# Performance work log

Measured on AMD Instinct MI355X. Metric: run time of the kernel, lower is better.

Reference implementation:

```python
import jax, jax.numpy as jnp
import numpy as np

# --- constants from loss_param_dict (fallback norm_info: means=0, stds=1 -> denorm is identity) ---
A_DIV, A_NS, A_BC = 0.3, 0.3, 0.3
A_LOSS = 1.0 - A_DIV - A_NS - A_BC
SCALE_BASE, SCALE_DIV, SCALE_NS, SCALE_BC = 300000.0, 1e-05, 0.01, 1.0
SX, SY = 1.2 / 127, 0.8 / 127  # spacing along axis 2 (x) and axis 1 (y)
RHO, MU = 1.0, 1.0
H, W = 128, 128
IN_TOP = H // 2 + H // 16 + 1  # 73
IN_BOT = H // 2 - H // 16 - 1  # 55
NORM_MEAN = np.array([0.0, 0.0, 0.0, 0.0], dtype=np.float32)
NORM_STD = np.array([1.0, 1.0, 1.0, 1.0], dtype=np.float32)


def grad_axis(f, h, axis):
    """torch.gradient: 2nd-order central interior, 1st-order one-sided edges."""
    f = jnp.moveaxis(f, axis, -1)
    left = (f[..., 1:2] - f[..., 0:1]) / h
    interior = (f[..., 2:] - f[..., :-2]) / (2.0 * h)
    right = (f[..., -1:] - f[..., -2:-1]) / h
    g = jnp.concatenate([left, interior, right], axis=-1)
    return jnp.moveaxis(g, -1, axis)


def setup_inputs() -> dict:
    key = jax.random.key(0)
    k1, k2, k3 = jax.random.split(key, 3)
    B = 256
    return {
        "inputs": jax.random.normal(k1, (B, 1, H, W), dtype=jnp.float32),
        "outputs": jax.random.normal(k2, (B, 3, H, W), dtype=jnp.float32),
        "targets": jax.random.normal(k3, (B, 3, H, W), dtype=jnp.float32),
    }


def reference(inputs, outputs, targets):
    # base MSE loss (reduction='sum')
    loss_base = jnp.sum((outputs - targets) ** 2) / SCALE_BASE

    # denormalisation (norm_info fallback: identity, but kept for faithfulness)
    in_ch = inputs.shape[1]
    mean = jnp.asarray(NORM_MEAN)
    std = jnp.asarray(NORM_STD)
    inp = inputs * std[:in_ch][None, :, None, None] + mean[:in_ch][None, :, None, None]
    out = outputs * std[in_ch:][None, :, None, None] + mean[in_ch:][None, :, None, None]

    # boundary residual pieces (on full, un-cropped denormalised outputs)
    pieces = [
        out[:, 1, IN_BOT:IN_TOP, 0].ravel() - 0.01,
        out[:, 0, IN_BOT:IN_TOP, -1].ravel(),
    ]
    for ch in (1, 2):
        for idx in (0, -1):
            pieces += [
                out[:, ch, idx, :].ravel(),
                out[:, ch, IN_TOP:, idx].ravel(),
                out[:, ch, 0:IN_BOT, idx].ravel(),
            ]
    boundary = jnp.concatenate(pieces)

    # interior crop [B, C, 126, 126]
    i_loc = inp[:, :, 1 : H - 1, 1 : W - 1]
    o_loc = out[:, :, 1 : H - 1, 1 : W - 1]

    p, u, v = o_loc[:, 0], o_loc[:, 1], o_loc[:, 2]  # [B,126,126]
    alpha = i_loc[:, 0]

    dp_dx, dp_dy = grad_axis(p, SX, 2), grad_axis(p, SY, 1)
    du_dx, du_dy = grad_axis(u, SX, 2), grad_axis(u, SY, 1)
    dv_dx, dv_dy = grad_axis(v, SX, 2), grad_axis(v, SY, 1)
    du_dxx = grad_axis(du_dx, SX, 2)
    du_dyy = grad_axis(du_dy, SY, 1)
    dv_dxx = grad_axis(dv_dx, SX, 2)
    dv_dyy = grad_axis(dv_dy, SY, 1)

    # continuity residual
    loss_cont = jnp.mean((du_dx + dv_dy) ** 2) / SCALE_DIV

    # Navier-Stokes residual
    x_res = u * du_dx + v * du_dy + dp_dx / RHO - MU * (du_dxx + du_dyy) / RHO + alpha * u / RHO
    y_res = u * dv_dx + v * dv_dy + dp_dy / RHO - MU * (dv_dxx + dv_dyy) / RHO + alpha * v / RHO
    mse_ns = (jnp.mean(x_res**2, axis=(1, 2)) + jnp.mean(y_res**2, axis=(1, 2))).mean() / 2.0
    loss_ns = mse_ns / SCALE_NS

    # boundary residual
    loss_bc = jnp.mean(boundary**2) / SCALE_BC

    return A_LOSS * loss_base + A_DIV * loss_cont + A_NS * loss_ns + A_BC * loss_bc
```

## Files before the change

kernel.cpp:

```cpp
#include <hip/hip_runtime.h>


#define HH 128
#define WW 128
#define NI 126
#define NBLK 4096

template <int I> __device__ __forceinline__ float gc(const float4& f) {
    if constexpr (I == 0) return f.x;
    else if constexpr (I == 1) return f.y;
    else if constexpr (I == 2) return f.z;
    else return f.w;
}

template <int IDX>
__device__ __forceinline__ float xsel(const float4& l, const float4& m, const float4& r) {
    if constexpr (IDX < 4) return gc<IDX>(l);
    else if constexpr (IDX < 8) return gc<IDX - 4>(m);
    else return gc<IDX - 8>(r);
}

__device__ __forceinline__ float grad1s(float m1, float a0, float p1, int i,
                                        float inv_h, float inv_2h) {
    if (i == 0) return (p1 - a0) * inv_h;
    if (i == NI - 1) return (a0 - m1) * inv_h;
    return (p1 - m1) * inv_2h;
}

__device__ __forceinline__ float grad2s(float m2, float m1, float a0, float p1, float p2,
                                        int i, float inv_h, float inv_2h) {
    if (i == 0) {
        const float d1 = (p2 - a0) * inv_2h, d0 = (p1 - a0) * inv_h;
        return (d1 - d0) * inv_h;
    }
    if (i == 1) {
        const float d1 = (p2 - a0) * inv_2h, dm1 = (a0 - m1) * inv_h;
        return (d1 - dm1) * inv_2h;
    }
    if (i == NI - 1) {
        const float d0 = (a0 - m1) * inv_h, dm1 = (a0 - m2) * inv_2h;
        return (d0 - dm1) * inv_h;
    }
    if (i == NI - 2) {
        const float d1 = (p1 - a0) * inv_h, dm1 = (a0 - m2) * inv_2h;
        return (d1 - dm1) * inv_2h;
    }
    return (p2 - 2.f * a0 + m2) * inv_2h * inv_2h;
}

struct Acc { float base, bc, cont, ns; };

template <int Q>
__device__ __forceinline__ void do_pixel(
    int r, int c0, bool midrow,
    const float4& uxl, const float4& uxm, const float4& uxr,
    const float4& uym2, const float4& uym1, const float4& uyp1, const float4& uyp2,
    const float4& vxl, const float4& vxm, const float4& vxr,
    const float4& vym2, const float4& vym1, const float4& vyp1, const float4& vyp2,
    const float4& pxl, const float4& pxm, const float4& pxr,
    const float4& pym1, const float4& pyp1,
    const float4& t0, const float4& t1, const float4& t2, const float4& av,
    Acc& acc) {
    const int c = c0 + Q;
    const float u0 = xsel<Q + 4>(uxl, uxm, uxr);
    const float v0 = xsel<Q + 4>(vxl, vxm, vxr);
    const float p0 = xsel<Q + 4>(pxl, pxm, pxr);

    {
        const float d0 = p0 - gc<Q>(t0);
        const float d1 = u0 - gc<Q>(t1);
        const float d2 = v0 - gc<Q>(t2);
        acc.base += d0 * d0 + d1 * d1 + d2 * d2;
    }
    if (c == 0 && midrow) { const float d = u0 - 0.01f; acc.bc += d * d; }
    if (c == WW - 1 && midrow) { acc.bc += p0 * p0; }
    if (r == 0 || r == HH - 1) { acc.bc += u0 * u0 + v0 * v0; }
    if ((c == 0 || c == WW - 1) && !midrow) { acc.bc += u0 * u0 + v0 * v0; }

    if (r >= 1 && r <= HH - 2 && c >= 1 && c <= WW - 2) {
        const int ic = c - 1, ir = r - 1;
        const float inv_sx = 127.0f / 1.2f, inv_2sx = 127.0f / 2.4f;
        const float inv_sy = 127.0f / 0.8f, inv_2sy = 127.0f / 1.6f;

        const float uxm2 = xsel<Q + 2>(uxl, uxm, uxr), uxm1 = xsel<Q + 3>(uxl, uxm, uxr);
        const float uxp1 = xsel<Q + 5>(uxl, uxm, uxr), uxp2 = xsel<Q + 6>(uxl, uxm, uxr);
        const float vxm2 = xsel<Q + 2>(vxl, vxm, vxr), vxm1 = xsel<Q + 3>(vxl, vxm, vxr);
        const float vxp1 = xsel<Q + 5>(vxl, vxm, vxr), vxp2 = xsel<Q + 6>(vxl, vxm, vxr);
        const float pxm1 = xsel<Q + 3>(pxl, pxm, pxr), pxp1 = xsel<Q + 5>(pxl, pxm, pxr);
        const float uym2s = gc<Q>(uym2), uym1s = gc<Q>(uym1);
        const float uyp1s = gc<Q>(uyp1), uyp2s = gc<Q>(uyp2);
        const float vym2s = gc<Q>(vym2), vym1s = gc<Q>(vym1);
        const float vyp1s = gc<Q>(vyp1), vyp2s = gc<Q>(vyp2);
        const float pym1s = gc<Q>(pym1), pyp1s = gc<Q>(pyp1);

        const float du_dx = grad1s(uxm1, u0, uxp1, ic, inv_sx, inv_2sx);
        const float du_dy = grad1s(uym1s, u0, uyp1s, ir, inv_sy, inv_2sy);
        const float dv_dx = grad1s(vxm1, v0, vxp1, ic, inv_sx, inv_2sx);
        const float dv_dy = grad1s(vym1s, v0, vyp1s, ir, inv_sy, inv_2sy);
        const float dp_dx = grad1s(pxm1, p0, pxp1, ic, inv_sx, inv_2sx);
        const float dp_dy = grad1s(pym1s, p0, pyp1s, ir, inv_sy, inv_2sy);
        const float du_dxx = grad2s(uxm2, uxm1, u0, uxp1, uxp2, ic, inv_sx, inv_2sx);
        const float du_dyy = grad2s(uym2s, uym1s, u0, uyp1s, uyp2s, ir, inv_sy, inv_2sy);
        const float dv_dxx = grad2s(vxm2, vxm1, v0, vxp1, vxp2, ic, inv_sx, inv_2sx);
        const float dv_dyy = grad2s(vym2s, vym1s, v0, vyp1s, vyp2s, ir, inv_sy, inv_2sy);

        const float alpha = gc<Q>(av);
        const float dvg = du_dx + dv_dy;
        acc.cont += dvg * dvg;
        const float xr_ = u0 * du_dx + v0 * du_dy + dp_dx - (du_dxx + du_dyy) + alpha * u0;
        const float yr_ = u0 * dv_dx + v0 * dv_dy + dp_dy - (dv_dxx + dv_dyy) + alpha * v0;
        acc.ns += xr_ * xr_ + yr_ * yr_;
    }
}

__global__ __launch_bounds__(256) void physics_loss_kernel(
    const float* __restrict__ inp, const float* __restrict__ out,
    const float* __restrict__ tgt, double* __restrict__ ws) {
    const int tid = threadIdx.x;
    const int grp = tid & 31;
    const int rloc = tid >> 5;
    const int bid = blockIdx.x;
    const int b = bid >> 4;
    const int r = ((bid & 15) << 3) | rloc;
    const int c0 = grp << 2;

    const float* O = out + (size_t)b * 3 * HH * WW;
    const float* T = tgt + (size_t)b * 3 * HH * WW;
    const float* A = inp + (size_t)b * HH * WW;
    const float* P = O;
    const float* U = O + HH * WW;
    const float* V = O + 2 * HH * WW;

    const int gl = grp == 0 ? 0 : grp - 1;
    const int gr = grp == 31 ? 31 : grp + 1;
    const int rm2 = r < 2 ? 0 : r - 2;
    const int rm1 = r < 1 ? 0 : r - 1;
    const int rp1 = r > 126 ? 127 : r + 1;
    const int rp2 = r > 125 ? 127 : r + 2;

    auto ld = [&](const float* base, int row, int gg) {
        return reinterpret_cast<const float4*>(base + row * WW)[gg];
    };

    const float4 uxl = ld(U, r, gl), uxm = ld(U, r, grp), uxr = ld(U, r, gr);
    const float4 uym2 = ld(U, rm2, grp), uym1 = ld(U, rm1, grp);
    const float4 uyp1 = ld(U, rp1, grp), uyp2 = ld(U, rp2, grp);
    const float4 vxl = ld(V, r, gl), vxm = ld(V, r, grp), vxr = ld(V, r, gr);
    const float4 vym2 = ld(V, rm2, grp), vym1 = ld(V, rm1, grp);
    const float4 vyp1 = ld(V, rp1, grp), vyp2 = ld(V, rp2, grp);
    const float4 pxl = ld(P, r, gl), pxm = ld(P, r, grp), pxr = ld(P, r, gr);
    const float4 pym1 = ld(P, rm1, grp), pyp1 = ld(P, rp1, grp);
    const float4 t0 = ld(T, r, grp);
    const float4 t1 = ld(T + HH * WW, r, grp);
    const float4 t2 = ld(T + 2 * HH * WW, r, grp);
    const float4 av = ld(A, r, grp);

    const bool midrow = (r >= 55 && r < 73);
    Acc acc = {0.f, 0.f, 0.f, 0.f};

    do_pixel<0>(r, c0, midrow, uxl, uxm, uxr, uym2, uym1, uyp1, uyp2,
                vxl, vxm, vxr, vym2, vym1, vyp1, vyp2,
                pxl, pxm, pxr, pym1, pyp1, t0, t1, t2, av, acc);
    do_pixel<1>(r, c0, midrow, uxl, uxm, uxr, uym2, uym1, uyp1, uyp2,
                vxl, vxm, vxr, vym2, vym1, vyp1, vyp2,
                pxl, pxm, pxr, pym1, pyp1, t0, t1, t2, av, acc);
    do_pixel<2>(r, c0, midrow, uxl, uxm, uxr, uym2, uym1, uyp1, uyp2,
                vxl, vxm, vxr, vym2, vym1, vyp1, vyp2,
                pxl, pxm, pxr, pym1, pyp1, t0, t1, t2, av, acc);
    do_pixel<3>(r, c0, midrow, uxl, uxm, uxr, uym2, uym1, uyp1, uyp2,
                vxl, vxm, vxr, vym2, vym1, vyp1, vyp2,
                pxl, pxm, pxr, pym1, pyp1, t0, t1, t2, av, acc);

    double a_base = acc.base, a_bc = acc.bc, a_cont = acc.cont, a_ns = acc.ns;
    #pragma unroll
    for (int off = 32; off > 0; off >>= 1) {
        a_base += __shfl_down(a_base, off);
        a_bc   += __shfl_down(a_bc, off);
        a_cont += __shfl_down(a_cont, off);
        a_ns   += __shfl_down(a_ns, off);
    }
    __shared__ double red[4][4];
    const int wave = tid >> 6, lane = tid & 63;
    if (lane == 0) {
        red[wave][0] = a_base; red[wave][1] = a_bc;
        red[wave][2] = a_cont; red[wave][3] = a_ns;
    }
    __syncthreads();
    if (tid == 0) {
        double b0 = 0, b1 = 0, b2 = 0, b3 = 0;
        #pragma unroll
        for (int w = 0; w < 4; ++w) {
            b0 += red[w][0]; b1 += red[w][1]; b2 += red[w][2]; b3 += red[w][3];
        }
        double* slot = ws + (size_t)blockIdx.x * 4;
        slot[0] = b0; slot[1] = b1; slot[2] = b2; slot[3] = b3;
    }
}

__global__ __launch_bounds__(256) void finalize_kernel(const double* __restrict__ ws,
                                                       float* __restrict__ out) {
    const int tid = threadIdx.x;
    double a0 = 0, a1 = 0, a2 = 0, a3 = 0;
    for (int b = tid; b < NBLK; b += 256) {
        const double* p = ws + (size_t)b * 4;
        a0 += p[0]; a1 += p[1]; a2 += p[2]; a3 += p[3];
    }
    #pragma unroll
    for (int off = 32; off > 0; off >>= 1) {
        a0 += __shfl_down(a0, off);
        a1 += __shfl_down(a1, off);
        a2 += __shfl_down(a2, off);
        a3 += __shfl_down(a3, off);
    }
    __shared__ double red[4][4];
    const int wave = tid >> 6, lane = tid & 63;
    if (lane == 0) {
        red[wave][0] = a0; red[wave][1] = a1; red[wave][2] = a2; red[wave][3] = a3;
    }
    __syncthreads();
    if (tid == 0) {
        double b0 = 0, b1 = 0, b2 = 0, b3 = 0;
        #pragma unroll
        for (int w = 0; w < 4; ++w) {
            b0 += red[w][0]; b1 += red[w][1]; b2 += red[w][2]; b3 += red[w][3];
        }
        const double loss_base = b0 / 300000.0;
        const double loss_cont = b2 / (256.0 * 126.0 * 126.0) / 1e-5;
        const double loss_ns   = b3 / (2.0 * 256.0 * 126.0 * 126.0) / 0.01;
        const double loss_bc   = b1 / (256.0 * 988.0);
        out[0] = (float)(0.10000000000000009 * loss_base +
                         0.3 * (loss_cont + loss_ns + loss_bc));
    }
}

extern "C" void kernel_launch(void* const* d_in, const int* in_sizes, int n_in,
                              void* d_out, int out_size, void* d_ws, size_t ws_size,
                              hipStream_t stream) {
    const float* inp = (const float*)d_in[0];
    const float* out = (const float*)d_in[1];
    const float* tgt = (const float*)d_in[2];
    float* o = (float*)d_out;
    double* ws = (double*)d_ws;

    hipLaunchKernelGGL(physics_loss_kernel, dim3(NBLK), dim3(256), 0, stream,
                       inp, out, tgt, ws);
    hipLaunchKernelGGL(finalize_kernel, dim3(1), dim3(256), 0, stream, ws, o);
}
```

Measured before the change: 33.41 us.

## Replace redundant stencil loads with wave shuffles and remap blocks across XCDs

Horizontal neighbour loads and one of the adjacent-row loads are now taken from other lanes of the same wave through shuffles, because each 64-lane wave covers two consecutive rows. This replaces many global/L2 float4 loads with cross-lane data movement. Block indices are also permuted so that consecutive logical blocks land on the same XCD, which should improve L2 reuse of the halo rows. The in-wave reduction moves from double to float, which is cheaper but slightly less precise.

```diff
diff --git a/kernel.cpp b/kernel.cpp
--- a/kernel.cpp
+++ b/kernel.cpp
@@ -113,16 +113,33 @@
     }
 }
 
+__device__ __forceinline__ float4 shf4(const float4& f, int src) {
+    float4 r;
+    r.x = __shfl(f.x, src, 64);
+    r.y = __shfl(f.y, src, 64);
+    r.z = __shfl(f.z, src, 64);
+    r.w = __shfl(f.w, src, 64);
+    return r;
+}
+
+__device__ __forceinline__ float4 sel4(bool c, const float4& a, const float4& b) {
+    float4 r;
+    r.x = c ? a.x : b.x; r.y = c ? a.y : b.y;
+    r.z = c ? a.z : b.z; r.w = c ? a.w : b.w;
+    return r;
+}
+
 __global__ __launch_bounds__(256) void physics_loss_kernel(
     const float* __restrict__ inp, const float* __restrict__ out,
     const float* __restrict__ tgt, double* __restrict__ ws) {
     const int tid = threadIdx.x;
     const int grp = tid & 31;
     const int rloc = tid >> 5;
-    const int bid = blockIdx.x;
+    const int bid = ((blockIdx.x & 7) << 9) | (blockIdx.x >> 3);
     const int b = bid >> 4;
     const int r = ((bid & 15) << 3) | rloc;
     const int c0 = grp << 2;
+    const int lane = tid & 63;
 
     const float* O = out + (size_t)b * 3 * HH * WW;
     const float* T = tgt + (size_t)b * 3 * HH * WW;
@@ -131,30 +148,44 @@
     const float* U = O + HH * WW;
     const float* V = O + 2 * HH * WW;
 
-    const int gl = grp == 0 ? 0 : grp - 1;
-    const int gr = grp == 31 ? 31 : grp + 1;
     const int rm2 = r < 2 ? 0 : r - 2;
     const int rm1 = r < 1 ? 0 : r - 1;
     const int rp1 = r > 126 ? 127 : r + 1;
     const int rp2 = r > 125 ? 127 : r + 2;
+    const bool evenRow = (lane < 32);
+    const int rOther = evenRow ? rm1 : rp1;
 
     auto ld = [&](const float* base, int row, int gg) {
         return reinterpret_cast<const float4*>(base + row * WW)[gg];
     };
 
-    const float4 uxl = ld(U, r, gl), uxm = ld(U, r, grp), uxr = ld(U, r, gr);
-    const float4 uym2 = ld(U, rm2, grp), uym1 = ld(U, rm1, grp);
-    const float4 uyp1 = ld(U, rp1, grp), uyp2 = ld(U, rp2, grp);
-    const float4 vxl = ld(V, r, gl), vxm = ld(V, r, grp), vxr = ld(V, r, gr);
-    const float4 vym2 = ld(V, rm2, grp), vym1 = ld(V, rm1, grp);
-    const float4 vyp1 = ld(V, rp1, grp), vyp2 = ld(V, rp2, grp);
-    const float4 pxl = ld(P, r, gl), pxm = ld(P, r, grp), pxr = ld(P, r, gr);
-    const float4 pym1 = ld(P, rm1, grp), pyp1 = ld(P, rp1, grp);
+    const float4 uxm = ld(U, r, grp);
+    const float4 uym2 = ld(U, rm2, grp), uoth = ld(U, rOther, grp), uyp2 = ld(U, rp2, grp);
+    const float4 vxm = ld(V, r, grp);
+    const float4 vym2 = ld(V, rm2, grp), voth = ld(V, rOther, grp), vyp2 = ld(V, rp2, grp);
+    const float4 pxm = ld(P, r, grp);
+    const float4 poth = ld(P, rOther, grp);
     const float4 t0 = ld(T, r, grp);
     const float4 t1 = ld(T + HH * WW, r, grp);
     const float4 t2 = ld(T + 2 * HH * WW, r, grp);
     const float4 av = ld(A, r, grp);
 
+    const int srcL = (lane & 32) | (grp == 0 ? 0 : grp - 1);
+    const int srcR = (lane & 32) | (grp == 31 ? 31 : grp + 1);
+    const int srcP = lane ^ 32;
+    const float4 uxl = shf4(uxm, srcL), uxr = shf4(uxm, srcR);
+    const float4 vxl = shf4(vxm, srcL), vxr = shf4(vxm, srcR);
+    const float4 pxl = shf4(pxm, srcL), pxr = shf4(pxm, srcR);
+    const float4 upart = shf4(uxm, srcP);
+    const float4 vpart = shf4(vxm, srcP);
+    const float4 ppart = shf4(pxm, srcP);
+    const float4 uym1 = sel4(evenRow, uoth, upart);
+    const float4 uyp1 = sel4(evenRow, upart, uoth);
+    const float4 vym1 = sel4(evenRow, voth, vpart);
+    const float4 vyp1 = sel4(evenRow, vpart, voth);
+    const float4 pym1 = sel4(evenRow, poth, ppart);
+    const float4 pyp1 = sel4(evenRow, ppart, poth);
+
     const bool midrow = (r >= 55 && r < 73);
     Acc acc = {0.f, 0.f, 0.f, 0.f};
 
@@ -171,7 +202,7 @@
                 vxl, vxm, vxr, vym2, vym1, vyp1, vyp2,
                 pxl, pxm, pxr, pym1, pyp1, t0, t1, t2, av, acc);
 
-    double a_base = acc.base, a_bc = acc.bc, a_cont = acc.cont, a_ns = acc.ns;
+    float a_base = acc.base, a_bc = acc.bc, a_cont = acc.cont, a_ns = acc.ns;
     #pragma unroll
     for (int off = 32; off > 0; off >>= 1) {
         a_base += __shfl_down(a_base, off);
@@ -179,8 +210,8 @@
         a_cont += __shfl_down(a_cont, off);
         a_ns   += __shfl_down(a_ns, off);
     }
-    __shared__ double red[4][4];
-    const int wave = tid >> 6, lane = tid & 63;
+    __shared__ float red[4][4];
+    const int wave = tid >> 6;
     if (lane == 0) {
         red[wave][0] = a_base; red[wave][1] = a_bc;
         red[wave][2] = a_cont; red[wave][3] = a_ns;
@@ -192,7 +223,7 @@
         for (int w = 0; w < 4; ++w) {
             b0 += red[w][0]; b1 += red[w][1]; b2 += red[w][2]; b3 += red[w][3];
         }
-        double* slot = ws + (size_t)blockIdx.x * 4;
+        double* slot = ws + (size_t)bid * 4;
         slot[0] = b0; slot[1] = b1; slot[2] = b2; slot[3] = b3;
     }
 }
```

Measured after the change: 34.74 us. +4.0%, slower.

## Stage stencil rows in LDS, swizzle block order, use float wave reductions

Applied to the files above, without the earlier changes.

Each block now cooperatively loads its 8-row strip of U, V and P plus halo rows into a shared-memory tile with coalesced float4 loads. Threads then read the stencil neighbours from LDS instead of issuing many redundant global loads per thread. Block indices are remapped so the eight XCD-interleaved blocks work on different batch regions, aiming at better L2 locality. The wave-level reductions switch from double to float shuffles, which are cheaper but slightly less precise.

```diff
diff --git a/kernel.cpp b/kernel.cpp
--- a/kernel.cpp
+++ b/kernel.cpp
@@ -119,9 +119,10 @@
     const int tid = threadIdx.x;
     const int grp = tid & 31;
     const int rloc = tid >> 5;
-    const int bid = blockIdx.x;
+    const int bid = ((blockIdx.x & 7) << 9) | (blockIdx.x >> 3);
     const int b = bid >> 4;
-    const int r = ((bid & 15) << 3) | rloc;
+    const int r0 = (bid & 15) << 3;
+    const int r = r0 | rloc;
     const int c0 = grp << 2;
 
     const float* O = out + (size_t)b * 3 * HH * WW;
@@ -131,29 +132,53 @@
     const float* U = O + HH * WW;
     const float* V = O + 2 * HH * WW;
 
-    const int gl = grp == 0 ? 0 : grp - 1;
-    const int gr = grp == 31 ? 31 : grp + 1;
-    const int rm2 = r < 2 ? 0 : r - 2;
-    const int rm1 = r < 1 ? 0 : r - 1;
-    const int rp1 = r > 126 ? 127 : r + 1;
-    const int rp2 = r > 125 ? 127 : r + 2;
-
+    __shared__ float4 stile[34][32];
+    float4 vals[5];
+    #pragma unroll
+    for (int k = 0; k < 5; ++k) {
+        if (k < 4 || tid < 64) {
+            const int i = tid + k * 256;
+            const int row = i >> 5, g = i & 31;
+            const float* base;
+            int rr;
+            if (row < 12)      { base = U; rr = r0 - 2 + row; }
+            else if (row < 24) { base = V; rr = r0 - 2 + (row - 12); }
+            else               { base = P; rr = r0 - 1 + (row - 24); }
+            rr = rr < 0 ? 0 : (rr > 127 ? 127 : rr);
+            vals[k] = *reinterpret_cast<const float4*>(base + rr * WW + g * 4);
+        }
+    }
     auto ld = [&](const float* base, int row, int gg) {
         return reinterpret_cast<const float4*>(base + row * WW)[gg];
     };
-
-    const float4 uxl = ld(U, r, gl), uxm = ld(U, r, grp), uxr = ld(U, r, gr);
-    const float4 uym2 = ld(U, rm2, grp), uym1 = ld(U, rm1, grp);
-    const float4 uyp1 = ld(U, rp1, grp), uyp2 = ld(U, rp2, grp);
-    const float4 vxl = ld(V, r, gl), vxm = ld(V, r, grp), vxr = ld(V, r, gr);
-    const float4 vym2 = ld(V, rm2, grp), vym1 = ld(V, rm1, grp);
-    const float4 vyp1 = ld(V, rp1, grp), vyp2 = ld(V, rp2, grp);
-    const float4 pxl = ld(P, r, gl), pxm = ld(P, r, grp), pxr = ld(P, r, gr);
-    const float4 pym1 = ld(P, rm1, grp), pyp1 = ld(P, rp1, grp);
     const float4 t0 = ld(T, r, grp);
     const float4 t1 = ld(T + HH * WW, r, grp);
     const float4 t2 = ld(T + 2 * HH * WW, r, grp);
     const float4 av = ld(A, r, grp);
+    __builtin_amdgcn_sched_barrier(0);
+    #pragma unroll
+    for (int k = 0; k < 5; ++k) {
+        if (k < 4 || tid < 64) {
+            const int i = tid + k * 256;
+            reinterpret_cast<float4*>(stile)[i] = vals[k];
+        }
+    }
+    __syncthreads();
+
+    const int gl = grp == 0 ? 0 : grp - 1;
+    const int gr = grp == 31 ? 31 : grp + 1;
+    const float4 uym2 = stile[rloc][grp],     uym1 = stile[rloc + 1][grp];
+    const float4 uxl  = stile[rloc + 2][gl],  uxm  = stile[rloc + 2][grp];
+    const float4 uxr  = stile[rloc + 2][gr];
+    const float4 uyp1 = stile[rloc + 3][grp], uyp2 = stile[rloc + 4][grp];
+    const float4 vym2 = stile[12 + rloc][grp],     vym1 = stile[12 + rloc + 1][grp];
+    const float4 vxl  = stile[12 + rloc + 2][gl],  vxm  = stile[12 + rloc + 2][grp];
+    const float4 vxr  = stile[12 + rloc + 2][gr];
+    const float4 vyp1 = stile[12 + rloc + 3][grp], vyp2 = stile[12 + rloc + 4][grp];
+    const float4 pym1 = stile[24 + rloc][grp];
+    const float4 pxl  = stile[24 + rloc + 1][gl],  pxm  = stile[24 + rloc + 1][grp];
+    const float4 pxr  = stile[24 + rloc + 1][gr];
+    const float4 pyp1 = stile[24 + rloc + 2][grp];
 
     const bool midrow = (r >= 55 && r < 73);
     Acc acc = {0.f, 0.f, 0.f, 0.f};
@@ -171,7 +196,7 @@
                 vxl, vxm, vxr, vym2, vym1, vyp1, vyp2,
                 pxl, pxm, pxr, pym1, pyp1, t0, t1, t2, av, acc);
 
-    double a_base = acc.base, a_bc = acc.bc, a_cont = acc.cont, a_ns = acc.ns;
+    float a_base = acc.base, a_bc = acc.bc, a_cont = acc.cont, a_ns = acc.ns;
     #pragma unroll
     for (int off = 32; off > 0; off >>= 1) {
         a_base += __shfl_down(a_base, off);
@@ -179,7 +204,7 @@
         a_cont += __shfl_down(a_cont, off);
         a_ns   += __shfl_down(a_ns, off);
     }
-    __shared__ double red[4][4];
+    __shared__ float red[4][4];
     const int wave = tid >> 6, lane = tid & 63;
     if (lane == 0) {
         red[wave][0] = a_base; red[wave][1] = a_bc;
@@ -192,7 +217,7 @@
         for (int w = 0; w < 4; ++w) {
             b0 += red[w][0]; b1 += red[w][1]; b2 += red[w][2]; b3 += red[w][3];
         }
-        double* slot = ws + (size_t)blockIdx.x * 4;
+        double* slot = ws + (size_t)bid * 4;
         slot[0] = b0; slot[1] = b1; slot[2] = b2; slot[3] = b3;
     }
 }
```

New measurement: 46.30 us. +38.6%, slower.
